# Kernel tuning notes

Measured on AMD Instinct MI355X. Metric: run time of the kernel, lower is better.

## Reference

```python
import jax, jax.numpy as jnp
import numpy as np
import math

N_HEAD = 12


def setup_inputs() -> dict:
    key = jax.random.key(0)
    ks = jax.random.split(key, 4)
    B, T, C = 8, 1024, 768
    s = 0.02
    return {
        "x": jax.random.normal(ks[0], (B, T, C), dtype=jnp.float32),
        "attn_mask": jnp.ones((B, T), dtype=jnp.int32),
        "W_attn": jax.random.normal(ks[1], (C, 3 * C), dtype=jnp.float32) * s,
        "b_attn": jnp.zeros((3 * C,), dtype=jnp.float32),
        "W_proj": jax.random.normal(ks[2], (C, C), dtype=jnp.float32) * s,
        "b_proj": jnp.zeros((C,), dtype=jnp.float32),
    }


def reference(x, attn_mask, W_attn, b_attn, W_proj, b_proj):
    B, T, C = x.shape
    hd = C // N_HEAD
    qkv = x @ W_attn + b_attn                      # [B, T, 3C]
    q, k, v = jnp.split(qkv, 3, axis=2)
    # [B, H, T, hd]
    q = q.reshape(B, T, N_HEAD, hd).transpose(0, 2, 1, 3)
    k = k.reshape(B, T, N_HEAD, hd).transpose(0, 2, 1, 3)
    v = v.reshape(B, T, N_HEAD, hd).transpose(0, 2, 1, 3)
    scores = jnp.einsum("bhqd,bhkd->bhqk", q, k) * (1.0 / math.sqrt(hd))
    mask = attn_mask[:, None, None, :]             # [B, 1, 1, T] broadcast over H, q
    scores = jnp.where(mask == 0, -jnp.inf, scores)
    attn = jax.nn.softmax(scores, axis=-1)
    out = jnp.einsum("bhqk,bhkd->bhqd", attn, v)   # [B, H, T, hd]
    out = out.transpose(0, 2, 1, 3).reshape(B, T, C)
    return out @ W_proj + b_proj
```

## Files before the change

### kernel.cpp

```cpp
#include <hip/hip_runtime.h>
#include <math.h>

constexpr int Bsz  = 8;
constexpr int Tseq = 1024;
constexpr int Cdim = 768;
constexpr int NH   = 12;
constexpr int HD   = 64;
constexpr int Mrows = Bsz * Tseq;
constexpr int C3    = 3 * Cdim;

using short8  = __attribute__((ext_vector_type(8))) short;
using s4v     = __attribute__((ext_vector_type(4))) short;
using floatx4 = __attribute__((ext_vector_type(4))) float;

__device__ __forceinline__ unsigned short f32_to_bf16_rn(float f) {
    unsigned int u = __float_as_uint(f);
    unsigned int r = u + 0x7FFFu + ((u >> 16) & 1u);
    return (unsigned short)(r >> 16);
}
__device__ __forceinline__ short8 lds_ld8(const unsigned short* p) {
    s4v a = *(const s4v*)p;
    s4v b = *(const s4v*)(p + 4);
    return __builtin_shufflevector(a, b, 0, 1, 2, 3, 4, 5, 6, 7);
}
__device__ __forceinline__ void lds_st8(unsigned short* p, short8 v) {
    *(s4v*)p       = __builtin_shufflevector(v, v, 0, 1, 2, 3);
    *(s4v*)(p + 4) = __builtin_shufflevector(v, v, 4, 5, 6, 7);
}

#define GLOAD_LDS16(g, l) __builtin_amdgcn_global_load_lds(                    \
    (const __attribute__((address_space(1))) void*)(g),                        \
    (__attribute__((address_space(3))) void*)(l), 16, 0, 0)

__global__ __launch_bounds__(256)
void to_bf16(const float* __restrict__ in, unsigned short* __restrict__ out, int n4)
{
    int t = blockIdx.x * blockDim.x + threadIdx.x;
    if (t >= n4) return;
    float4 v = ((const float4*)in)[t];
    ushort4 o;
    o.x = f32_to_bf16_rn(v.x);
    o.y = f32_to_bf16_rn(v.y);
    o.z = f32_to_bf16_rn(v.z);
    o.w = f32_to_bf16_rn(v.w);
    ((ushort4*)out)[t] = o;
}

__global__ __launch_bounds__(256)
void transpose_bf16(const float* __restrict__ in, unsigned short* __restrict__ out,
                    int K, int N)
{
    __shared__ float tile[32][33];
    const int k0 = blockIdx.y * 32, n0 = blockIdx.x * 32;
    const int tx = threadIdx.x & 31, ty = threadIdx.x >> 5;
    #pragma unroll
    for (int r = ty; r < 32; r += 8)
        tile[r][tx] = in[(size_t)(k0 + r) * N + n0 + tx];
    __syncthreads();
    #pragma unroll
    for (int r = ty; r < 32; r += 8)
        out[(size_t)(n0 + r) * K + k0 + tx] = f32_to_bf16_rn(tile[tx][r]);
}

__global__ __launch_bounds__(256)
void gemm_qkv(const unsigned short* __restrict__ A_g,
              const unsigned short* __restrict__ B_g,
              const float* __restrict__ bias,
              unsigned short* __restrict__ Cb,
              int M, int N, int K)
{
    __shared__ __align__(16) unsigned short Ah[2][128 * 32];
    __shared__ __align__(16) unsigned short Bh[2][128 * 32];

    const int tid  = threadIdx.x;
    const int wave = tid >> 6;
    const int lane = tid & 63;
    const int lm   = lane & 15;
    const int quad = lane >> 4;
    const int wy   = wave >> 1, wx = wave & 1;
    const int row0 = blockIdx.y * 128;
    const int col0 = blockIdx.x * 128;

    const int sr  = lane >> 2;
    const int skp = (lane & 3) * 8;
    const int NI  = K / 32;

    floatx4 acc[4][4] = {};

    #pragma unroll
    for (int s = 0; s < 2; ++s) {
        const int r = (wave * 2 + s) * 16 + sr;
        GLOAD_LDS16(A_g + (size_t)(row0 + r) * K + skp, &Ah[0][r * 32 + skp]);
        GLOAD_LDS16(B_g + (size_t)(col0 + r) * K + skp, &Bh[0][r * 32 + skp]);
    }
    __syncthreads();

    for (int kt = 0; kt < NI; ++kt) {
        const int cur = kt & 1, nxt = cur ^ 1;

        if (kt + 1 < NI) {
            const int k0 = (kt + 1) * 32;
            #pragma unroll
            for (int s = 0; s < 2; ++s) {
                const int r = (wave * 2 + s) * 16 + sr;
                GLOAD_LDS16(A_g + (size_t)(row0 + r) * K + k0 + skp, &Ah[nxt][r * 32 + skp]);
                GLOAD_LDS16(B_g + (size_t)(col0 + r) * K + k0 + skp, &Bh[nxt][r * 32 + skp]);
            }
        }

        short8 af[4];
        #pragma unroll
        for (int i = 0; i < 4; ++i)
            af[i] = *(const short8*)&Ah[cur][(wy * 64 + i * 16 + lm) * 32 + quad * 8];
        #pragma unroll
        for (int j = 0; j < 4; ++j) {
            short8 bf = *(const short8*)&Bh[cur][(wx * 64 + j * 16 + lm) * 32 + quad * 8];
            #pragma unroll
            for (int i = 0; i < 4; ++i)
                acc[i][j] = __builtin_amdgcn_mfma_f32_16x16x32_bf16(af[i], bf, acc[i][j], 0, 0, 0);
        }

        __syncthreads();
    }

    unsigned short* wbuf = &Ah[0][wave * 1024];
    #pragma unroll
    for (int i = 0; i < 4; ++i) {
        #pragma unroll
        for (int j = 0; j < 4; ++j) {
            const float bv = bias[col0 + wx * 64 + j * 16 + lm];
            #pragma unroll
            for (int r = 0; r < 4; ++r)
                wbuf[(quad * 4 + r) * 64 + j * 16 + lm] = f32_to_bf16_rn(acc[i][j][r] + bv);
        }
        asm volatile("s_waitcnt lgkmcnt(0)" ::: "memory");
        #pragma unroll
        for (int p = 0; p < 2; ++p) {
            const int lrow  = p * 8 + (lane >> 3);
            const int lcol8 = (lane & 7) * 8;
            short8 v = lds_ld8(&wbuf[lrow * 64 + lcol8]);
            *(short8*)(Cb + (size_t)(row0 + wy * 64 + i * 16 + lrow) * N +
                       col0 + wx * 64 + lcol8) = v;
        }
        asm volatile("s_waitcnt lgkmcnt(0)" ::: "memory");
    }
}

__global__ __launch_bounds__(256)
void gemm_proj(const unsigned short* __restrict__ AO_g,
               const unsigned short* __restrict__ B_g,
               const float* __restrict__ bias,
               float* __restrict__ C,
               int M, int N, int K)
{
    __shared__ __align__(16) unsigned short Ah[2][128 * 32];
    __shared__ __align__(16) unsigned short Bh[2][128 * 32];

    const int tid  = threadIdx.x;
    const int wave = tid >> 6;
    const int lane = tid & 63;
    const int lm   = lane & 15;
    const int quad = lane >> 4;
    const int wy   = wave >> 1, wx = wave & 1;
    const int row0 = blockIdx.y * 128;
    const int col0 = blockIdx.x * 128;

    const int sr  = lane >> 2;
    const int skp = (lane & 3) * 8;
    const int NI  = K / 32;

    floatx4 acc[4][4] = {};

    {
        const int head0 = skp >> 6, off0 = skp & 63;
        #pragma unroll
        for (int s = 0; s < 2; ++s) {
            const int r = (wave * 2 + s) * 16 + sr;
            GLOAD_LDS16(AO_g + (size_t)head0 * (Mrows * HD) + (size_t)(row0 + r) * HD + off0,
                        &Ah[0][r * 32 + skp]);
            GLOAD_LDS16(B_g + (size_t)(col0 + r) * K + skp, &Bh[0][r * 32 + skp]);
        }
    }
    __syncthreads();

    for (int kt = 0; kt < NI; ++kt) {
        const int cur = kt & 1, nxt = cur ^ 1;

        if (kt + 1 < NI) {
            const int k0   = (kt + 1) * 32;
            const int kk   = k0 + skp;
            const int head = kk >> 6;
            const int off  = kk & 63;
            #pragma unroll
            for (int s = 0; s < 2; ++s) {
                const int r = (wave * 2 + s) * 16 + sr;
                GLOAD_LDS16(AO_g + (size_t)head * (Mrows * HD) + (size_t)(row0 + r) * HD + off,
                            &Ah[nxt][r * 32 + skp]);
                GLOAD_LDS16(B_g + (size_t)(col0 + r) * K + k0 + skp, &Bh[nxt][r * 32 + skp]);
            }
        }

        short8 af[4];
        #pragma unroll
        for (int i = 0; i < 4; ++i)
            af[i] = *(const short8*)&Ah[cur][(wy * 64 + i * 16 + lm) * 32 + quad * 8];
        #pragma unroll
        for (int j = 0; j < 4; ++j) {
            short8 bf = *(const short8*)&Bh[cur][(wx * 64 + j * 16 + lm) * 32 + quad * 8];
            #pragma unroll
            for (int i = 0; i < 4; ++i)
                acc[i][j] = __builtin_amdgcn_mfma_f32_16x16x32_bf16(af[i], bf, acc[i][j], 0, 0, 0);
        }

        __syncthreads();
    }

    #pragma unroll
    for (int j = 0; j < 4; ++j) {
        const int col = col0 + wx * 64 + j * 16 + lm;
        const float bv = bias[col];
        #pragma unroll
        for (int i = 0; i < 4; ++i) {
            const int rowb = row0 + wy * 64 + i * 16 + quad * 4;
            #pragma unroll
            for (int r = 0; r < 4; ++r)
                C[(size_t)(rowb + r) * N + col] = acc[i][j][r] + bv;
        }
    }
}

__global__ __launch_bounds__(256, 2)
void attn_bf16(const unsigned short* __restrict__ qkv,
               const int* __restrict__ mask,
               unsigned short* __restrict__ outh)
{
    constexpr int LDW = 68;
    constexpr int NT  = Tseq / 64;
    __shared__ __align__(16) unsigned short Kh[2][64 * LDW];
    __shared__ __align__(16) unsigned short Vh[2][64 * LDW];
    __shared__ __align__(16) unsigned short Ph[128 * LDW];
    __shared__ float maskadd[2][64];

    const int tid  = threadIdx.x;
    const int wave = tid >> 6;
    const int lane = tid & 63;
    const int lm   = lane & 15;
    const int quad = lane >> 4;
    const int idx  = blockIdx.x;
    const int bh   = idx % (Bsz * NH);
    const int qb   = idx / (Bsz * NH);
    const int b    = bh / NH;
    const int h    = bh % NH;
    const int q0   = qb * 128;
    const float scale = 0.125f;

    short8 qf[2][2];
    #pragma unroll
    for (int mt = 0; mt < 2; ++mt) {
        const size_t qrow = (size_t)(b * Tseq + q0 + wave * 32 + mt * 16 + lm) * C3 + h * HD;
        #pragma unroll
        for (int kf = 0; kf < 2; ++kf)
            qf[mt][kf] = *(const short8*)(qkv + qrow + kf * 32 + quad * 8);
    }

    const int sr0 = (tid & 31) * 2;
    const int sc  = (tid >> 5) * 8;

    short8 kh0, kh1, vh0, vh1;
    float  mreg = 0.f;

    {
        const size_t g0 = (size_t)(b * Tseq + sr0) * C3 + Cdim + h * HD + sc;
        kh0 = *(const short8*)(qkv + g0);
        kh1 = *(const short8*)(qkv + g0 + C3);
        vh0 = *(const short8*)(qkv + g0 + Cdim);
        vh1 = *(const short8*)(qkv + g0 + Cdim + C3);
        if (tid < 64) mreg = (mask[b * Tseq + tid] == 0) ? -1e30f : 0.0f;
        lds_st8(&Kh[0][sr0 * LDW + sc], kh0);
        lds_st8(&Kh[0][(sr0 + 1) * LDW + sc], kh1);
        #pragma unroll
        for (int i = 0; i < 8; ++i) {
            unsigned int pv = (unsigned int)(unsigned short)vh0[i] |
                              ((unsigned int)(unsigned short)vh1[i] << 16);
            *(unsigned int*)&Vh[0][(sc + i) * LDW + sr0] = pv;
        }
        if (tid < 64) maskadd[0][tid] = mreg;
    }
    __syncthreads();

    floatx4 O[2][4] = {};
    float lsum[2] = {0.f, 0.f};
    float madd[4][4];

    for (int kt = 0; kt < NT; ++kt) {
        const int cur = kt & 1;
        const int nxt = cur ^ 1;
        const unsigned short* Khc = Kh[cur];
        const unsigned short* Vhc = Vh[cur];

        if (kt + 1 < NT) {
            const size_t g0 = (size_t)(b * Tseq + (kt + 1) * 64 + sr0) * C3 + Cdim + h * HD + sc;
            kh0 = *(const short8*)(qkv + g0);
            kh1 = *(const short8*)(qkv + g0 + C3);
            vh0 = *(const short8*)(qkv + g0 + Cdim);
            vh1 = *(const short8*)(qkv + g0 + Cdim + C3);
            if (tid < 64) mreg = (mask[b * Tseq + (kt + 1) * 64 + tid] == 0) ? -1e30f : 0.0f;
        }

        floatx4 S[2][4] = {};
        #pragma unroll
        for (int kf = 0; kf < 2; ++kf) {
            short8 kh[4];
            #pragma unroll
            for (int nt = 0; nt < 4; ++nt)
                kh[nt] = lds_ld8(&Khc[(nt * 16 + lm) * LDW + kf * 32 + quad * 8]);
            #pragma unroll
            for (int mt = 0; mt < 2; ++mt)
                #pragma unroll
                for (int nt = 0; nt < 4; ++nt)
                    S[mt][nt] = __builtin_amdgcn_mfma_f32_16x16x32_bf16(kh[nt], qf[mt][kf], S[mt][nt], 0, 0, 0);
        }
        #pragma unroll
        for (int nt = 0; nt < 4; ++nt)
            #pragma unroll
            for (int r = 0; r < 4; ++r)
                madd[nt][r] = maskadd[cur][nt * 16 + quad * 4 + r];

        #pragma unroll
        for (int mt = 0; mt < 2; ++mt) {
            const int prow = (wave * 32 + mt * 16 + lm) * LDW;
            #pragma unroll
            for (int nt = 0; nt < 4; ++nt) {
                ushort4 pk;
                unsigned short* pp = &pk.x;
                #pragma unroll
                for (int r = 0; r < 4; ++r) {
                    float p = __expf(S[mt][nt][r] * scale + madd[nt][r]);
                    lsum[mt] += p;
                    pp[r] = f32_to_bf16_rn(p);
                }
                *(ushort4*)&Ph[prow + nt * 16 + quad * 4] = pk;
            }
        }

        #pragma unroll
        for (int kf = 0; kf < 2; ++kf) {
            short8 pf[2];
            #pragma unroll
            for (int mt = 0; mt < 2; ++mt)
                pf[mt] = lds_ld8(&Ph[(wave * 32 + mt * 16 + lm) * LDW + kf * 32 + quad * 8]);
            #pragma unroll
            for (int dt = 0; dt < 4; ++dt) {
                short8 vh = lds_ld8(&Vhc[(dt * 16 + lm) * LDW + kf * 32 + quad * 8]);
                #pragma unroll
                for (int mt = 0; mt < 2; ++mt)
                    O[mt][dt] = __builtin_amdgcn_mfma_f32_16x16x32_bf16(vh, pf[mt], O[mt][dt], 0, 0, 0);
            }
        }

        if (kt + 1 < NT) {
            lds_st8(&Kh[nxt][sr0 * LDW + sc], kh0);
            lds_st8(&Kh[nxt][(sr0 + 1) * LDW + sc], kh1);
            #pragma unroll
            for (int i = 0; i < 8; ++i) {
                unsigned int pv = (unsigned int)(unsigned short)vh0[i] |
                                  ((unsigned int)(unsigned short)vh1[i] << 16);
                *(unsigned int*)&Vh[nxt][(sc + i) * LDW + sr0] = pv;
            }
            if (tid < 64) maskadd[nxt][tid] = mreg;
        }
        __syncthreads();
    }

    #pragma unroll
    for (int mt = 0; mt < 2; ++mt) {
        lsum[mt] += __shfl_xor(lsum[mt], 16);
        lsum[mt] += __shfl_xor(lsum[mt], 32);
        const float inv_l = 1.0f / lsum[mt];
        const size_t row = (size_t)h * (Mrows * HD) +
                           (size_t)(b * Tseq + q0 + wave * 32 + mt * 16 + lm) * HD;
        #pragma unroll
        for (int dt = 0; dt < 4; ++dt) {
            ushort4 hv;
            unsigned short* hp = &hv.x;
            #pragma unroll
            for (int r = 0; r < 4; ++r)
                hp[r] = f32_to_bf16_rn(O[mt][dt][r] * inv_l);
            *(ushort4*)(outh + row + dt * 16 + quad * 4) = hv;
        }
    }
}

extern "C" void kernel_launch(void* const* d_in, const int* in_sizes, int n_in,
                              void* d_out, int out_size, void* d_ws, size_t ws_size,
                              hipStream_t stream)
{
    const float* x      = (const float*)d_in[0];
    const int*   mask   = (const int*)  d_in[1];
    const float* W_attn = (const float*)d_in[2];
    const float* b_attn = (const float*)d_in[3];
    const float* W_proj = (const float*)d_in[4];
    const float* b_proj = (const float*)d_in[5];
    float* out = (float*)d_out;

    unsigned short* xh    = (unsigned short*)d_ws;
    unsigned short* wat_h = xh    + (size_t)Mrows * Cdim;
    unsigned short* wpt_h = wat_h + (size_t)C3 * Cdim;
    unsigned short* qkvh  = wpt_h + (size_t)Cdim * Cdim;
    unsigned short* aoh   = xh;

    dim3 blk(256);

    to_bf16<<<dim3(Mrows * Cdim / 4 / 256), blk, 0, stream>>>(x, xh, Mrows * Cdim / 4);
    transpose_bf16<<<dim3(C3 / 32, Cdim / 32), blk, 0, stream>>>(W_attn, wat_h, Cdim, C3);
    transpose_bf16<<<dim3(Cdim / 32, Cdim / 32), blk, 0, stream>>>(W_proj, wpt_h, Cdim, Cdim);

    gemm_qkv<<<dim3(C3 / 128, Mrows / 128), blk, 0, stream>>>(
        xh, wat_h, b_attn, qkvh, Mrows, C3, Cdim);

    attn_bf16<<<dim3((Tseq / 128) * Bsz * NH), blk, 0, stream>>>(qkvh, mask, aoh);

    gemm_proj<<<dim3(Cdim / 128, Mrows / 128), blk, 0, stream>>>(
        aoh, wpt_h, b_proj, out, Mrows, Cdim, Cdim);
}
```

Before: 210.9 us.

## Enlarge GEMM tiles to 256x128 with triple-buffered swizzled LDS and XCD-aware block mapping

Both GEMMs (QKV and output projection) now use 256x128 tiles, so each wave owns 8x4 MFMA accumulators instead of 4x4. Operands are staged through a three-deep LDS ring with vmcnt-based waits and a single barrier per k-step, replacing the double buffer with a barrier at both ends. LDS columns are XOR-swizzled to avoid bank conflicts, blocks are remapped across the 8 XCDs, and MFMA sections run at raised wave priority. The aim is higher arithmetic intensity and better latency hiding, at the cost of more registers and LDS per block and fewer blocks in flight.

```diff
diff --git a/kernel.cpp b/kernel.cpp
--- a/kernel.cpp
+++ b/kernel.cpp
@@ -31,6 +31,9 @@
 #define GLOAD_LDS16(g, l) __builtin_amdgcn_global_load_lds(                    \
     (const __attribute__((address_space(1))) void*)(g),                        \
     (__attribute__((address_space(3))) void*)(l), 16, 0, 0)
+
+#define WAITVM6 asm volatile("s_waitcnt vmcnt(6)" ::: "memory")
+#define WAITVM0 asm volatile("s_waitcnt vmcnt(0)" ::: "memory")
 
 __global__ __launch_bounds__(256)
 void to_bf16(const float* __restrict__ in, unsigned short* __restrict__ out, int n4)
@@ -62,15 +65,16 @@
         out[(size_t)(n0 + r) * K + k0 + tx] = f32_to_bf16_rn(tile[tx][r]);
 }
 
-__global__ __launch_bounds__(256)
+__global__ __launch_bounds__(256, 2)
 void gemm_qkv(const unsigned short* __restrict__ A_g,
               const unsigned short* __restrict__ B_g,
               const float* __restrict__ bias,
               unsigned short* __restrict__ Cb,
               int M, int N, int K)
 {
-    __shared__ __align__(16) unsigned short Ah[2][128 * 32];
-    __shared__ __align__(16) unsigned short Bh[2][128 * 32];
+    constexpr int BM = 256, BN = 128, BK = 32;
+    __shared__ __align__(16) unsigned short Ah[3][BM * BK];
+    __shared__ __align__(16) unsigned short Bh[3][BN * BK];
 
     const int tid  = threadIdx.x;
     const int wave = tid >> 6;
@@ -78,60 +82,80 @@
     const int lm   = lane & 15;
     const int quad = lane >> 4;
     const int wy   = wave >> 1, wx = wave & 1;
-    const int row0 = blockIdx.y * 128;
-    const int col0 = blockIdx.x * 128;
-
-    const int sr  = lane >> 2;
-    const int skp = (lane & 3) * 8;
-    const int NI  = K / 32;
-
-    floatx4 acc[4][4] = {};
-
-    #pragma unroll
-    for (int s = 0; s < 2; ++s) {
-        const int r = (wave * 2 + s) * 16 + sr;
-        GLOAD_LDS16(A_g + (size_t)(row0 + r) * K + skp, &Ah[0][r * 32 + skp]);
-        GLOAD_LDS16(B_g + (size_t)(col0 + r) * K + skp, &Bh[0][r * 32 + skp]);
-    }
-    __syncthreads();
-
+
+    const int nby = M / BM;
+    const int nwg = (N / BN) * nby;
+    const int sid = (blockIdx.x & 7) * (nwg >> 3) + (blockIdx.x >> 3);
+    const int by  = sid & (nby - 1);
+    const int bx  = sid / nby;
+    const int row0 = by * BM, col0 = bx * BN;
+    const int NI  = K / BK;
+
+    const int sq8 = (quad ^ ((lm ^ (lm >> 2)) & 3)) * 8;
+
+    floatx4 acc[8][4] = {};
+
+    auto stage = [&](int buf, int k0) {
+        #pragma unroll
+        for (int s4 = 0; s4 < 4; ++s4) {
+            const int c = s4 * 256 + tid;
+            const int r = c >> 2, q = c & 3;
+            const int col = (q ^ ((r ^ (r >> 2)) & 3)) * 8;
+            GLOAD_LDS16(A_g + (size_t)(row0 + r) * K + k0 + col, &Ah[buf][c * 8]);
+        }
+        #pragma unroll
+        for (int s2 = 0; s2 < 2; ++s2) {
+            const int c = s2 * 256 + tid;
+            const int r = c >> 2, q = c & 3;
+            const int col = (q ^ ((r ^ (r >> 2)) & 3)) * 8;
+            GLOAD_LDS16(B_g + (size_t)(col0 + r) * K + k0 + col, &Bh[buf][c * 8]);
+        }
+    };
+
+    stage(0, 0);
+    stage(1, BK);
+
+    int cur = 0;
     for (int kt = 0; kt < NI; ++kt) {
-        const int cur = kt & 1, nxt = cur ^ 1;
-
-        if (kt + 1 < NI) {
-            const int k0 = (kt + 1) * 32;
-            #pragma unroll
-            for (int s = 0; s < 2; ++s) {
-                const int r = (wave * 2 + s) * 16 + sr;
-                GLOAD_LDS16(A_g + (size_t)(row0 + r) * K + k0 + skp, &Ah[nxt][r * 32 + skp]);
-                GLOAD_LDS16(B_g + (size_t)(col0 + r) * K + k0 + skp, &Bh[nxt][r * 32 + skp]);
-            }
-        }
-
-        short8 af[4];
-        #pragma unroll
-        for (int i = 0; i < 4; ++i)
-            af[i] = *(const short8*)&Ah[cur][(wy * 64 + i * 16 + lm) * 32 + quad * 8];
+        if (kt < NI - 1) { WAITVM6; } else { WAITVM0; }
+        __builtin_amdgcn_s_barrier();
+        asm volatile("" ::: "memory");
+
+        if (kt + 2 < NI) {
+            int stg = cur + 2; if (stg >= 3) stg -= 3;
+            stage(stg, (kt + 2) * BK);
+        }
+
+        short8 af[8];
+        #pragma unroll
+        for (int i = 0; i < 8; ++i)
+            af[i] = *(const short8*)&Ah[cur][(wy * 128 + i * 16 + lm) * BK + sq8];
+
+        __builtin_amdgcn_s_setprio(1);
         #pragma unroll
         for (int j = 0; j < 4; ++j) {
-            short8 bf = *(const short8*)&Bh[cur][(wx * 64 + j * 16 + lm) * 32 + quad * 8];
-            #pragma unroll
-            for (int i = 0; i < 4; ++i)
+            short8 bf = *(const short8*)&Bh[cur][(wx * 64 + j * 16 + lm) * BK + sq8];
+            #pragma unroll
+            for (int i = 0; i < 8; ++i)
                 acc[i][j] = __builtin_amdgcn_mfma_f32_16x16x32_bf16(af[i], bf, acc[i][j], 0, 0, 0);
         }
-
-        __syncthreads();
-    }
+        __builtin_amdgcn_s_setprio(0);
+
+        cur = (cur == 2) ? 0 : cur + 1;
+    }
+
+    float bvj[4];
+    #pragma unroll
+    for (int j = 0; j < 4; ++j) bvj[j] = bias[col0 + wx * 64 + j * 16 + lm];
 
     unsigned short* wbuf = &Ah[0][wave * 1024];
     #pragma unroll
-    for (int i = 0; i < 4; ++i) {
+    for (int i = 0; i < 8; ++i) {
         #pragma unroll
         for (int j = 0; j < 4; ++j) {
-            const float bv = bias[col0 + wx * 64 + j * 16 + lm];
             #pragma unroll
             for (int r = 0; r < 4; ++r)
-                wbuf[(quad * 4 + r) * 64 + j * 16 + lm] = f32_to_bf16_rn(acc[i][j][r] + bv);
+                wbuf[(quad * 4 + r) * 64 + j * 16 + lm] = f32_to_bf16_rn(acc[i][j][r] + bvj[j]);
         }
         asm volatile("s_waitcnt lgkmcnt(0)" ::: "memory");
         #pragma unroll
@@ -139,22 +163,23 @@
             const int lrow  = p * 8 + (lane >> 3);
             const int lcol8 = (lane & 7) * 8;
             short8 v = lds_ld8(&wbuf[lrow * 64 + lcol8]);
-            *(short8*)(Cb + (size_t)(row0 + wy * 64 + i * 16 + lrow) * N +
+            *(short8*)(Cb + (size_t)(row0 + wy * 128 + i * 16 + lrow) * N +
                        col0 + wx * 64 + lcol8) = v;
         }
         asm volatile("s_waitcnt lgkmcnt(0)" ::: "memory");
     }
 }
 
-__global__ __launch_bounds__(256)
+__global__ __launch_bounds__(256, 2)
 void gemm_proj(const unsigned short* __restrict__ AO_g,
                const unsigned short* __restrict__ B_g,
                const float* __restrict__ bias,
                float* __restrict__ C,
                int M, int N, int K)
 {
-    __shared__ __align__(16) unsigned short Ah[2][128 * 32];
-    __shared__ __align__(16) unsigned short Bh[2][128 * 32];
+    constexpr int BM = 256, BN = 128, BK = 32;
+    __shared__ __align__(16) unsigned short Ah[3][BM * BK];
+    __shared__ __align__(16) unsigned short Bh[3][BN * BK];
 
     const int tid  = threadIdx.x;
     const int wave = tid >> 6;
@@ -162,57 +187,69 @@
     const int lm   = lane & 15;
     const int quad = lane >> 4;
     const int wy   = wave >> 1, wx = wave & 1;
-    const int row0 = blockIdx.y * 128;
-    const int col0 = blockIdx.x * 128;
-
-    const int sr  = lane >> 2;
-    const int skp = (lane & 3) * 8;
-    const int NI  = K / 32;
-
-    floatx4 acc[4][4] = {};
-
-    {
-        const int head0 = skp >> 6, off0 = skp & 63;
-        #pragma unroll
-        for (int s = 0; s < 2; ++s) {
-            const int r = (wave * 2 + s) * 16 + sr;
-            GLOAD_LDS16(AO_g + (size_t)head0 * (Mrows * HD) + (size_t)(row0 + r) * HD + off0,
-                        &Ah[0][r * 32 + skp]);
-            GLOAD_LDS16(B_g + (size_t)(col0 + r) * K + skp, &Bh[0][r * 32 + skp]);
-        }
-    }
-    __syncthreads();
-
+
+    const int nby = M / BM;
+    const int nwg = (N / BN) * nby;
+    const int sid = (blockIdx.x & 7) * (nwg >> 3) + (blockIdx.x >> 3);
+    const int by  = sid & (nby - 1);
+    const int bx  = sid / nby;
+    const int row0 = by * BM, col0 = bx * BN;
+    const int NI  = K / BK;
+
+    const int sq8 = (quad ^ ((lm ^ (lm >> 2)) & 3)) * 8;
+
+    floatx4 acc[8][4] = {};
+
+    auto stage = [&](int buf, int k0) {
+        const int head = k0 >> 6;
+        const int offb = k0 & 63;
+        #pragma unroll
+        for (int s4 = 0; s4 < 4; ++s4) {
+            const int c = s4 * 256 + tid;
+            const int r = c >> 2, q = c & 3;
+            const int col = (q ^ ((r ^ (r >> 2)) & 3)) * 8;
+            GLOAD_LDS16(AO_g + (size_t)head * (Mrows * HD) +
+                        (size_t)(row0 + r) * HD + offb + col, &Ah[buf][c * 8]);
+        }
+        #pragma unroll
+        for (int s2 = 0; s2 < 2; ++s2) {
+            const int c = s2 * 256 + tid;
+            const int r = c >> 2, q = c & 3;
+            const int col = (q ^ ((r ^ (r >> 2)) & 3)) * 8;
+            GLOAD_LDS16(B_g + (size_t)(col0 + r) * K + k0 + col, &Bh[buf][c * 8]);
+        }
+    };
+
+    stage(0, 0);
+    stage(1, BK);
+
+    int cur = 0;
     for (int kt = 0; kt < NI; ++kt) {
-        const int cur = kt & 1, nxt = cur ^ 1;
-
-        if (kt + 1 < NI) {
-            const int k0   = (kt + 1) * 32;
-            const int kk   = k0 + skp;
-            const int head = kk >> 6;
-            const int off  = kk & 63;
-            #pragma unroll
-            for (int s = 0; s < 2; ++s) {
-                const int r = (wave * 2 + s) * 16 + sr;
-                GLOAD_LDS16(AO_g + (size_t)head * (Mrows * HD) + (size_t)(row0 + r) * HD + off,
-                            &Ah[nxt][r * 32 + skp]);
-                GLOAD_LDS16(B_g + (size_t)(col0 + r) * K + k0 + skp, &Bh[nxt][r * 32 + skp]);
-            }
-        }
-
-        short8 af[4];
-        #pragma unroll
-        for (int i = 0; i < 4; ++i)
-            af[i] = *(const short8*)&Ah[cur][(wy * 64 + i * 16 + lm) * 32 + quad * 8];
+        if (kt < NI - 1) { WAITVM6; } else { WAITVM0; }
+        __builtin_amdgcn_s_barrier();
+        asm volatile("" ::: "memory");
+
+        if (kt + 2 < NI) {
+            int stg = cur + 2; if (stg >= 3) stg -= 3;
+            stage(stg, (kt + 2) * BK);
+        }
+
+        short8 af[8];
+        #pragma unroll
+        for (int i = 0; i < 8; ++i)
+            af[i] = *(const short8*)&Ah[cur][(wy * 128 + i * 16 + lm) * BK + sq8];
+
+        __builtin_amdgcn_s_setprio(1);
         #pragma unroll
         for (int j = 0; j < 4; ++j) {
-            short8 bf = *(const short8*)&Bh[cur][(wx * 64 + j * 16 + lm) * 32 + quad * 8];
-            #pragma unroll
-            for (int i = 0; i < 4; ++i)
+            short8 bf = *(const short8*)&Bh[cur][(wx * 64 + j * 16 + lm) * BK + sq8];
+            #pragma unroll
+            for (int i = 0; i < 8; ++i)
                 acc[i][j] = __builtin_amdgcn_mfma_f32_16x16x32_bf16(af[i], bf, acc[i][j], 0, 0, 0);
         }
-
-        __syncthreads();
+        __builtin_amdgcn_s_setprio(0);
+
+        cur = (cur == 2) ? 0 : cur + 1;
     }
 
     #pragma unroll
@@ -220,8 +257,8 @@
         const int col = col0 + wx * 64 + j * 16 + lm;
         const float bv = bias[col];
         #pragma unroll
-        for (int i = 0; i < 4; ++i) {
-            const int rowb = row0 + wy * 64 + i * 16 + quad * 4;
+        for (int i = 0; i < 8; ++i) {
+            const int rowb = row0 + wy * 128 + i * 16 + quad * 4;
             #pragma unroll
             for (int r = 0; r < 4; ++r)
                 C[(size_t)(rowb + r) * N + col] = acc[i][j][r] + bv;
@@ -415,11 +452,11 @@
     transpose_bf16<<<dim3(C3 / 32, Cdim / 32), blk, 0, stream>>>(W_attn, wat_h, Cdim, C3);
     transpose_bf16<<<dim3(Cdim / 32, Cdim / 32), blk, 0, stream>>>(W_proj, wpt_h, Cdim, Cdim);
 
-    gemm_qkv<<<dim3(C3 / 128, Mrows / 128), blk, 0, stream>>>(
+    gemm_qkv<<<dim3((C3 / 128) * (Mrows / 256)), blk, 0, stream>>>(
         xh, wat_h, b_attn, qkvh, Mrows, C3, Cdim);
 
     attn_bf16<<<dim3((Tseq / 128) * Bsz * NH), blk, 0, stream>>>(qkvh, mask, aoh);
 
-    gemm_proj<<<dim3(Cdim / 128, Mrows / 128), blk, 0, stream>>>(
+    gemm_proj<<<dim3((Cdim / 128) * (Mrows / 256)), blk, 0, stream>>>(
         aoh, wpt_h, b_proj, out, Mrows, Cdim, Cdim);
 }
```

New measurement: 228.5 us. 8.3% more time.

## Rewrite QKV GEMM with 256x256 tiles, 8 waves, triple-buffered LDS pipeline

Applied to the files above, without the earlier changes.

Replaces the 128x128, 4-wave QKV GEMM with a 512-thread kernel. It computes 256x256 tiles over most of the output plus a 128x128 tail for the remaining columns, giving 320 blocks in one launch with a swizzled block order. Loads go through a 3-stage LDS ring with XOR-swizzled columns to avoid bank conflicts. Explicit vmcnt waits, split MFMA phases with s_setprio, and a padded epilogue buffer aim to overlap global loads with matrix math and raise reuse per block. The cost is more register pressure at one block per CU and fragile hand-counted wait logic.

```diff
diff --git a/kernel.cpp b/kernel.cpp
--- a/kernel.cpp
+++ b/kernel.cpp
@@ -31,6 +31,8 @@
 #define GLOAD_LDS16(g, l) __builtin_amdgcn_global_load_lds(                    \
     (const __attribute__((address_space(1))) void*)(g),                        \
     (__attribute__((address_space(3))) void*)(l), 16, 0, 0)
+
+#define WAITVM0 asm volatile("s_waitcnt vmcnt(0)" ::: "memory")
 
 __global__ __launch_bounds__(256)
 void to_bf16(const float* __restrict__ in, unsigned short* __restrict__ out, int n4)
@@ -62,87 +64,151 @@
         out[(size_t)(n0 + r) * K + k0 + tx] = f32_to_bf16_rn(tile[tx][r]);
 }
 
-__global__ __launch_bounds__(256)
-void gemm_qkv(const unsigned short* __restrict__ A_g,
-              const unsigned short* __restrict__ B_g,
-              const float* __restrict__ bias,
-              unsigned short* __restrict__ Cb,
-              int M, int N, int K)
-{
-    __shared__ __align__(16) unsigned short Ah[2][128 * 32];
-    __shared__ __align__(16) unsigned short Bh[2][128 * 32];
+template<int MH>
+__device__ __forceinline__ void qkv_body(
+    const unsigned short* __restrict__ A_g,
+    const unsigned short* __restrict__ B_g,
+    const float* __restrict__ bias,
+    unsigned short* __restrict__ Cb,
+    const int row0, const int col0, const int K, const int N,
+    unsigned short* lds)
+{
+    constexpr int BK   = 32;
+    constexpr int BUFS = 16384;
 
     const int tid  = threadIdx.x;
     const int wave = tid >> 6;
     const int lane = tid & 63;
     const int lm   = lane & 15;
     const int quad = lane >> 4;
-    const int wy   = wave >> 1, wx = wave & 1;
-    const int row0 = blockIdx.y * 128;
-    const int col0 = blockIdx.x * 128;
-
-    const int sr  = lane >> 2;
-    const int skp = (lane & 3) * 8;
-    const int NI  = K / 32;
-
-    floatx4 acc[4][4] = {};
-
-    #pragma unroll
-    for (int s = 0; s < 2; ++s) {
-        const int r = (wave * 2 + s) * 16 + sr;
-        GLOAD_LDS16(A_g + (size_t)(row0 + r) * K + skp, &Ah[0][r * 32 + skp]);
-        GLOAD_LDS16(B_g + (size_t)(col0 + r) * K + skp, &Bh[0][r * 32 + skp]);
-    }
-    __syncthreads();
-
+    const int wy   = wave >> 2;
+    const int wx   = wave & 3;
+    const int NI   = K / BK;
+    const int sq8  = (quad ^ ((lm ^ (lm >> 2)) & 3)) * 8;
+    const int sr   = tid >> 2;
+    const int sq   = tid & 3;
+
+    floatx4 acc[4 * MH][4] = {};
+
+    auto stageA = [&](int buf, int k0, int h) {
+        const int r  = h * 128 + sr;
+        const int gc = k0 + ((sq ^ ((r ^ (r >> 2)) & 3)) << 3);
+        GLOAD_LDS16(A_g + (size_t)(row0 + r) * K + gc,
+                    lds + buf * BUFS + r * 32 + sq * 8);
+    };
+    auto stageB = [&](int buf, int k0, int h) {
+        const int r  = h * 128 + sr;
+        const int gc = k0 + ((sq ^ ((r ^ (r >> 2)) & 3)) << 3);
+        GLOAD_LDS16(B_g + (size_t)(col0 + r) * K + gc,
+                    lds + buf * BUFS + 8192 + r * 32 + sq * 8);
+    };
+
+    #pragma unroll
+    for (int h = 0; h < MH; ++h) stageA(0, 0, h);
+    stageB(0, 0, 0); stageB(0, 0, 1);
+    #pragma unroll
+    for (int h = 0; h < MH; ++h) stageA(1, BK, h);
+    stageB(1, BK, 0); stageB(1, BK, 1);
+    if constexpr (MH == 2) asm volatile("s_waitcnt vmcnt(4)" ::: "memory");
+    else                   asm volatile("s_waitcnt vmcnt(3)" ::: "memory");
+    __builtin_amdgcn_s_barrier();
+
+    short8 af[2 * MH], bf[4];
+    int cur = 0;
     for (int kt = 0; kt < NI; ++kt) {
-        const int cur = kt & 1, nxt = cur ^ 1;
-
-        if (kt + 1 < NI) {
-            const int k0 = (kt + 1) * 32;
-            #pragma unroll
-            for (int s = 0; s < 2; ++s) {
-                const int r = (wave * 2 + s) * 16 + sr;
-                GLOAD_LDS16(A_g + (size_t)(row0 + r) * K + k0 + skp, &Ah[nxt][r * 32 + skp]);
-                GLOAD_LDS16(B_g + (size_t)(col0 + r) * K + k0 + skp, &Bh[nxt][r * 32 + skp]);
-            }
-        }
-
-        short8 af[4];
-        #pragma unroll
-        for (int i = 0; i < 4; ++i)
-            af[i] = *(const short8*)&Ah[cur][(wy * 64 + i * 16 + lm) * 32 + quad * 8];
+        const unsigned short* bufA = lds + cur * BUFS;
+        const unsigned short* bufB = bufA + 8192;
+        const int  stg  = (cur + 2 >= 3) ? cur - 1 : cur + 2;
+        const int  k2   = (kt + 2) * BK;
+        const bool doSt = (kt + 2 < NI);
+
+        #pragma unroll
+        for (int u = 0; u < 2 * MH; ++u)
+            af[u] = *(const short8*)(bufA + (wy * (64 * MH) + u * 16 + lm) * 32 + sq8);
+        #pragma unroll
+        for (int j = 0; j < 4; ++j)
+            bf[j] = *(const short8*)(bufB + (wx * 64 + j * 16 + lm) * 32 + sq8);
+        if (doSt) {
+            stageA(stg, k2, 0);
+            if constexpr (MH == 2) stageA(stg, k2, 1); else stageB(stg, k2, 0);
+        }
+        __builtin_amdgcn_s_barrier();
+        __builtin_amdgcn_s_setprio(1);
+        #pragma unroll
+        for (int u = 0; u < 2 * MH; ++u)
+            #pragma unroll
+            for (int j = 0; j < 4; ++j)
+                acc[u][j] = __builtin_amdgcn_mfma_f32_16x16x32_bf16(af[u], bf[j], acc[u][j], 0, 0, 0);
+        __builtin_amdgcn_s_setprio(0);
+        __builtin_amdgcn_s_barrier();
+
+        #pragma unroll
+        for (int u = 0; u < 2 * MH; ++u)
+            af[u] = *(const short8*)(bufA + (wy * (64 * MH) + (2 * MH + u) * 16 + lm) * 32 + sq8);
+        if (doSt) {
+            if constexpr (MH == 2) { stageB(stg, k2, 0); stageB(stg, k2, 1); }
+            else                   stageB(stg, k2, 1);
+        }
+        __builtin_amdgcn_s_barrier();
+        __builtin_amdgcn_s_setprio(1);
+        #pragma unroll
+        for (int u = 0; u < 2 * MH; ++u)
+            #pragma unroll
+            for (int j = 0; j < 4; ++j)
+                acc[2 * MH + u][j] = __builtin_amdgcn_mfma_f32_16x16x32_bf16(af[u], bf[j], acc[2 * MH + u][j], 0, 0, 0);
+        __builtin_amdgcn_s_setprio(0);
+        if (kt == NI - 2) { WAITVM0; }
+        else if (kt < NI - 2) {
+            if constexpr (MH == 2) asm volatile("s_waitcnt vmcnt(4)" ::: "memory");
+            else                   asm volatile("s_waitcnt vmcnt(3)" ::: "memory");
+        }
+        __builtin_amdgcn_s_barrier();
+
+        cur = (cur == 2) ? 0 : cur + 1;
+    }
+    asm volatile("" ::: "memory");
+
+    unsigned short* wbuf = lds + (NI % 3) * BUFS + wave * 1088;
+    float bvj[4];
+    #pragma unroll
+    for (int j = 0; j < 4; ++j) bvj[j] = bias[col0 + wx * 64 + j * 16 + lm];
+    #pragma unroll
+    for (int i = 0; i < 4 * MH; ++i) {
         #pragma unroll
         for (int j = 0; j < 4; ++j) {
-            short8 bf = *(const short8*)&Bh[cur][(wx * 64 + j * 16 + lm) * 32 + quad * 8];
-            #pragma unroll
-            for (int i = 0; i < 4; ++i)
-                acc[i][j] = __builtin_amdgcn_mfma_f32_16x16x32_bf16(af[i], bf, acc[i][j], 0, 0, 0);
-        }
-
-        __syncthreads();
-    }
-
-    unsigned short* wbuf = &Ah[0][wave * 1024];
-    #pragma unroll
-    for (int i = 0; i < 4; ++i) {
-        #pragma unroll
-        for (int j = 0; j < 4; ++j) {
-            const float bv = bias[col0 + wx * 64 + j * 16 + lm];
             #pragma unroll
             for (int r = 0; r < 4; ++r)
-                wbuf[(quad * 4 + r) * 64 + j * 16 + lm] = f32_to_bf16_rn(acc[i][j][r] + bv);
+                wbuf[(quad * 4 + r) * 68 + j * 16 + lm] = f32_to_bf16_rn(acc[i][j][r] + bvj[j]);
         }
         asm volatile("s_waitcnt lgkmcnt(0)" ::: "memory");
         #pragma unroll
         for (int p = 0; p < 2; ++p) {
             const int lrow  = p * 8 + (lane >> 3);
             const int lcol8 = (lane & 7) * 8;
-            short8 v = lds_ld8(&wbuf[lrow * 64 + lcol8]);
-            *(short8*)(Cb + (size_t)(row0 + wy * 64 + i * 16 + lrow) * N +
+            short8 v = lds_ld8(&wbuf[lrow * 68 + lcol8]);
+            *(short8*)(Cb + (size_t)(row0 + wy * (64 * MH) + i * 16 + lrow) * N +
                        col0 + wx * 64 + lcol8) = v;
         }
         asm volatile("s_waitcnt lgkmcnt(0)" ::: "memory");
+    }
+}
+
+__global__ __launch_bounds__(512, 1)
+void gemm_qkv8p(const unsigned short* __restrict__ A_g,
+                const unsigned short* __restrict__ B_g,
+                const float* __restrict__ bias,
+                unsigned short* __restrict__ Cb)
+{
+    __shared__ __align__(16) unsigned short lds[3 * 16384];
+    const int bid = blockIdx.x;
+    if (bid < 256) {
+        const int sid = (bid & 7) * 32 + (bid >> 3);
+        qkv_body<2>(A_g, B_g, bias, Cb,
+                    (sid >> 3) * 256, (sid & 7) * 256, Cdim, C3, lds);
+    } else {
+        const int t   = bid - 256;
+        const int sid = (t & 7) * 8 + (t >> 3);
+        qkv_body<1>(A_g, B_g, bias, Cb, sid * 128, 2048, Cdim, C3, lds);
     }
 }
 
@@ -415,8 +481,7 @@
     transpose_bf16<<<dim3(C3 / 32, Cdim / 32), blk, 0, stream>>>(W_attn, wat_h, Cdim, C3);
     transpose_bf16<<<dim3(Cdim / 32, Cdim / 32), blk, 0, stream>>>(W_proj, wpt_h, Cdim, Cdim);
 
-    gemm_qkv<<<dim3(C3 / 128, Mrows / 128), blk, 0, stream>>>(
-        xh, wat_h, b_attn, qkvh, Mrows, C3, Cdim);
+    gemm_qkv8p<<<dim3(320), dim3(512), 0, stream>>>(xh, wat_h, b_attn, qkvh);
 
     attn_bf16<<<dim3((Tseq / 128) * Bsz * NH), blk, 0, stream>>>(qkvh, mask, aoh);
 
```

Result: no change. 207.3 us (-1.7%).
